# Kernel tuning notes

Hardware: AMD Instinct MI355X
Metric: run time of the kernel (lower is better)

## Reference

```python
import jax, jax.numpy as jnp
import numpy as np

B, L, H = 32, 2048, 512
EPS = 1e-6


def setup_inputs() -> dict:
    key = jax.random.key(0)
    k1, k2 = jax.random.split(key)
    hidden = jax.random.normal(k1, (B, L, H), dtype=jnp.float32)
    # nn.Linear(H, H): weight [H, H], bias [H]; use kaiming-uniform-like scale
    bound = 1.0 / np.sqrt(H)
    W = jax.random.uniform(k2, (H, H), dtype=jnp.float32, minval=-bound, maxval=bound)
    b = jnp.zeros((H,), dtype=jnp.float32)
    return {"hidden": hidden, "W": W, "b": b}


def reference(hidden, W, b):
    Bn, Ln, Hn = hidden.shape

    def step(M, k):
        # k: [B, H]; key == value == hidden[:, t, :]
        v_pred = jnp.einsum("bij,bj->bi", M, k)               # M @ k
        denom = jnp.sum(k * k, axis=-1, keepdims=True) + EPS   # [B, 1]
        delta_v = k - v_pred / denom                           # v - v_pred/denom (v == k)
        M = M + jnp.einsum("bi,bj->bij", delta_v, k)           # outer-product update
        return M, None

    M0 = jnp.zeros((Bn, Hn, Hn), dtype=hidden.dtype)
    xs = jnp.swapaxes(hidden[:, :-1, :], 0, 1)  # [L-1, B, H]
    M, _ = jax.lax.scan(step, M0, xs)

    query = hidden[:, -1, :]                                   # [B, H]
    context = jnp.einsum("bij,bj->bi", M, query)               # [B, H]
    return context @ W.T + b                                   # read_proj
```

## Files before the change

kernel.cpp:

```cpp
#include <hip/hip_runtime.h>
#include <hip/hip_fp16.h>

#define B_  32
#define L_  2048
#define H_  512
#define CA  64
#define NC  32
#define EPSF 1e-6f

typedef _Float16 f16x8 __attribute__((ext_vector_type(8)));
typedef float f32x16 __attribute__((ext_vector_type(16)));

template <int CTRL>
__device__ __forceinline__ float dpp_shift_add(float x) {
  int t = __builtin_amdgcn_update_dpp(0, __float_as_int(x), CTRL, 0xf, 0xf, true);
  return x + __int_as_float(t);
}
__device__ __forceinline__ float wave_reduce_lane63(float x) {
  x = dpp_shift_add<0x111>(x);
  x = dpp_shift_add<0x112>(x);
  x = dpp_shift_add<0x114>(x);
  x = dpp_shift_add<0x118>(x);
  x = dpp_shift_add<0x142>(x);
  x = dpp_shift_add<0x143>(x);
  return x;
}
__device__ __forceinline__ float row16_reduce(float x) {
  x = dpp_shift_add<0x111>(x);
  x = dpp_shift_add<0x112>(x);
  x = dpp_shift_add<0x114>(x);
  x = dpp_shift_add<0x118>(x);
  return x;
}
__device__ __forceinline__ float rdlane(float v, int l) {
  return __int_as_float(__builtin_amdgcn_readlane(__float_as_int(v), l));
}
__device__ __forceinline__ void unpack8(const uint4& k, float* f) {
  const float2 f0 = __half22float2(*(const __half2*)&k.x);
  const float2 f1 = __half22float2(*(const __half2*)&k.y);
  const float2 f2 = __half22float2(*(const __half2*)&k.z);
  const float2 f3 = __half22float2(*(const __half2*)&k.w);
  f[0] = f0.x; f[1] = f0.y; f[2] = f1.x; f[3] = f1.y;
  f[4] = f2.x; f[5] = f2.y; f[6] = f3.x; f[7] = f3.y;
}

#define KFI(row, k8) (((((row) * 64) + (k8)) * 8) ^ (((row) & 7) << 3))

__global__ __launch_bounds__(256) void
deltarule_gram64(const float* __restrict__ hidden,
                 unsigned short* __restrict__ Kh,
                 float* __restrict__ tmT, float* __restrict__ dvec) {
  const int cb = blockIdx.x, b = blockIdx.y;
  const int tid = threadIdx.x, lane = tid & 63, wv = tid >> 6;
  __shared__ __align__(16) unsigned short Kf[CA * H_];
  __shared__ __align__(16) float G[CA * CA];

  const int c0 = cb * CA;
  const float* src = hidden + ((size_t)b * L_ + c0) * H_;
  unsigned short* kout = Kh + ((size_t)b * L_ + c0) * H_;
  const bool lastc = (cb == NC - 1);

#pragma unroll
  for (int u = 0; u < 16; ++u) {
    const int f8 = u * 256 + tid;
    const int row = f8 >> 6;
    const int colf = (f8 & 63) * 8;
    float4 va = *(const float4*)(src + row * H_ + colf);
    float4 vb = *(const float4*)(src + row * H_ + colf + 4);
    if (lastc && row == CA - 1) {
      va = make_float4(0.f, 0.f, 0.f, 0.f);
      vb = make_float4(0.f, 0.f, 0.f, 0.f);
    }
    __half2 h0 = __floats2half2_rn(va.x, va.y);
    __half2 h1 = __floats2half2_rn(va.z, va.w);
    __half2 h2 = __floats2half2_rn(vb.x, vb.y);
    __half2 h3 = __floats2half2_rn(vb.z, vb.w);
    uint4 pk = make_uint4(*(unsigned int*)&h0, *(unsigned int*)&h1,
                          *(unsigned int*)&h2, *(unsigned int*)&h3);
    *(uint4*)&Kf[KFI(row, colf >> 3)] = pk;
    *(uint4*)(kout + row * H_ + colf) = pk;
  }
  __syncthreads();

  if (wv < 3) {
    const int ta = (wv == 2) ? 1 : 0;
    const int tb = (wv == 0) ? 0 : 1;
    const int mrow = 32 * ta + (lane & 31);
    const int nrow = 32 * tb + (lane & 31);
    const int khi = lane >> 5;
    f32x16 acc;
#pragma unroll
    for (int r = 0; r < 16; ++r) acc[r] = 0.f;
#pragma unroll
    for (int kk = 0; kk < 32; ++kk) {
      const int k8 = 2 * kk + khi;
      const f16x8 av = *(const f16x8*)&Kf[KFI(mrow, k8)];
      const f16x8 bv = *(const f16x8*)&Kf[KFI(nrow, k8)];
      acc = __builtin_amdgcn_mfma_f32_32x32x16_f16(av, bv, acc, 0, 0, 0);
    }
#pragma unroll
    for (int r = 0; r < 16; ++r) {
      const int row32 = (r & 3) + 8 * (r >> 2) + 4 * khi;
      G[(32 * ta + row32) * CA + 32 * tb + (lane & 31)] = acc[r];
    }
  }
  __syncthreads();

  if (tid < CA) dvec[((size_t)b * NC + cb) * CA + tid] = G[tid * CA + tid] + EPSF;
  __syncthreads();

  if (wv < 2) {
    const int off = wv * 32;
    const int j = lane & 31;
    float Gr[32], X[32];
#pragma unroll
    for (int t = 0; t < 32; ++t) Gr[t] = G[(off + t) * CA + off + j];
#pragma unroll
    for (int t = 31; t >= 0; --t) {
      float i0 = 0.f, i1 = 0.f;
#pragma unroll
      for (int s = t + 1; s < 32; s += 2) i0 = fmaf(rdlane(Gr[t], s), X[s], i0);
#pragma unroll
      for (int s = t + 2; s < 32; s += 2) i1 = fmaf(rdlane(Gr[t], s), X[s], i1);
      X[t] = (((j == t) ? 1.f : 0.f) - (i0 + i1)) / (rdlane(Gr[t], t) + EPSF);
    }
    if (lane < 32) {
#pragma unroll
      for (int t = 0; t < 32; ++t) G[(off + t) * CA + off + j] = X[t];
    }
  }
  __syncthreads();

  const int zr = tid >> 3;
  const int zc = (tid & 7) * 4;
  float4 zf = make_float4(0.f, 0.f, 0.f, 0.f);
#pragma unroll
  for (int s = 0; s < 32; ++s) {
    const float u = G[zr * CA + 32 + s];
    const float4 xv = *(const float4*)&G[(32 + s) * CA + 32 + zc];
    zf.x = fmaf(u, xv.x, zf.x); zf.y = fmaf(u, xv.y, zf.y);
    zf.z = fmaf(u, xv.z, zf.z); zf.w = fmaf(u, xv.w, zf.w);
  }
  __syncthreads();
  *(float4*)&G[zr * CA + 32 + zc] = zf;
  __syncthreads();
  float4 yf = make_float4(0.f, 0.f, 0.f, 0.f);
#pragma unroll
  for (int s = 0; s < 32; ++s) {
    const float u = G[zr * CA + s];
    const float4 zv = *(const float4*)&G[s * CA + 32 + zc];
    yf.x = fmaf(u, zv.x, yf.x); yf.y = fmaf(u, zv.y, yf.y);
    yf.z = fmaf(u, zv.z, yf.z); yf.w = fmaf(u, zv.w, yf.w);
  }
  __syncthreads();
  *(float4*)&G[zr * CA + 32 + zc] = make_float4(-yf.x, -yf.y, -yf.z, -yf.w);
  __syncthreads();

  float* tout = tmT + ((size_t)b * NC + cb) * (CA * CA);
#pragma unroll
  for (int v = 0; v < 4; ++v) {
    const int f4 = v * 256 + tid;
    const int s = f4 >> 4;
    const int j4 = (f4 & 15) * 4;
    float4 val;
    if (s >= 32 && j4 < 32) val = make_float4(0.f, 0.f, 0.f, 0.f);
    else                    val = *(const float4*)&G[s * CA + j4];
    *(float4*)(tout + s * CA + j4) = val;
  }
}

__global__ __launch_bounds__(1024) void
deltarule_scan64p(const float* __restrict__ hidden,
                  const unsigned short* __restrict__ Kh,
                  const float* __restrict__ Wm, const float* __restrict__ bias,
                  const float* __restrict__ tmT, const float* __restrict__ dvec,
                  float* __restrict__ out) {
  const int b = blockIdx.x, tid = threadIdx.x, lane = tid & 63, wv = tid >> 6;
  __shared__ __align__(16) float Wsw[H_];
  __shared__ __align__(16) float Ctx[H_];
  __shared__ __align__(16) float PartU[16 * 1024];
  __shared__ float Part2[64 * 17];

  const unsigned short* khb = Kh + (size_t)b * L_ * H_;
  const float* tmb = tmT + (size_t)b * NC * (CA * CA);
  const float* dvb = dvec + (size_t)b * NC * CA;

  const int job = 64 * wv + lane;

  if (tid < H_) {
    const float q = hidden[((size_t)b * L_ + (L_ - 1)) * H_ + tid];
    const int p = ((tid & 4) << 6) + ((tid >> 3) << 2) + (tid & 3);
    Wsw[p] = q;
  }
  float4 wq4 = make_float4(0.f, 0.f, 0.f, 0.f);
  float4 cq4 = make_float4(0.f, 0.f, 0.f, 0.f);
  if (wv < 2)
    wq4 = *(const float4*)(hidden + ((size_t)b * L_ + (L_ - 1)) * H_ + 4 * job);

  int cmbBase = 0;
  if (wv < 2)                 cmbBase = (job & 1) * 256 + (job >> 1) * 4;
  else if (wv < 4) { const int qc = job - 128;
                     cmbBase = 512 + (qc & 1) * 256 + (qc >> 1) * 4; }

  uint4 kr[4];
  float4 tA;
  float dv;
#pragma unroll
  for (int i = 0; i < 4; ++i)
    kr[i] = *(const uint4*)(khb + ((size_t)(NC - 1) * CA + 4 * wv + i) * H_ + 8 * lane);
  tA = *(const float4*)(tmb + (size_t)(NC - 1) * (CA * CA) + lane * CA + 4 * wv);
  dv = dvb[(NC - 1) * CA + lane];
  asm volatile("s_waitcnt vmcnt(0) lgkmcnt(0)\n\ts_barrier" ::: "memory");

  for (int c = NC - 1; c >= 0; --c) {
    uint4 kn[4];
    float4 nA;
    float dN = 0.f;
    if (c > 0) {
#pragma unroll
      for (int i = 0; i < 4; ++i)
        kn[i] = *(const uint4*)(khb + ((size_t)(c - 1) * CA + 4 * wv + i) * H_ + 8 * lane);
      nA = *(const float4*)(tmb + (size_t)(c - 1) * (CA * CA) + lane * CA + 4 * wv);
      dN = dvb[(c - 1) * CA + lane];
    }

    const float4 wa  = *(const float4*)&Wsw[4 * lane];
    const float4 wb2 = *(const float4*)&Wsw[256 + 4 * lane];
    float ysg[4];
#pragma unroll
    for (int i = 0; i < 4; ++i) {
      float kf[8];
      unpack8(kr[i], kf);
      float p = kf[0] * wa.x;
      p = fmaf(kf[1], wa.y, p);  p = fmaf(kf[2], wa.z, p);
      p = fmaf(kf[3], wa.w, p);  p = fmaf(kf[4], wb2.x, p);
      p = fmaf(kf[5], wb2.y, p); p = fmaf(kf[6], wb2.z, p);
      p = fmaf(kf[7], wb2.w, p);
      p = wave_reduce_lane63(p);
      ysg[i] = rdlane(p, 63);
    }

    float sp = ysg[0] * tA.x;
    sp = fmaf(ysg[1], tA.y, sp);
    sp = fmaf(ysg[2], tA.z, sp);
    sp = fmaf(ysg[3], tA.w, sp);
    Part2[lane * 17 + wv] = sp;
    asm volatile("s_waitcnt lgkmcnt(0)\n\ts_barrier" ::: "memory");

    float red = Part2[(4 * wv + (lane >> 4)) * 17 + (lane & 15)];
    red = row16_reduce(red);
    const float sg0 = rdlane(red, 15);
    const float sg1 = rdlane(red, 31);
    const float sg2 = rdlane(red, 47);
    const float sg3 = rdlane(red, 63);
    const float sv0 = sg0 * rdlane(dv, 4 * wv + 0);
    const float sv1 = sg1 * rdlane(dv, 4 * wv + 1);
    const float sv2 = sg2 * rdlane(dv, 4 * wv + 2);
    const float sv3 = sg3 * rdlane(dv, 4 * wv + 3);

    float ws[8] = {0,0,0,0,0,0,0,0}, cs[8] = {0,0,0,0,0,0,0,0};
#pragma unroll
    for (int i = 0; i < 4; ++i) {
      float kf[8];
      unpack8(kr[i], kf);
      const float sg = (i == 0) ? sg0 : (i == 1) ? sg1 : (i == 2) ? sg2 : sg3;
      const float sv = (i == 0) ? sv0 : (i == 1) ? sv1 : (i == 2) ? sv2 : sv3;
#pragma unroll
      for (int e = 0; e < 8; ++e) {
        ws[e] = fmaf(sg, kf[e], ws[e]);
        cs[e] = fmaf(sv, kf[e], cs[e]);
      }
    }
    {
      float* pw = &PartU[wv * 1024];
      *(float4*)&pw[4 * lane]       = make_float4(ws[0], ws[1], ws[2], ws[3]);
      *(float4*)&pw[256 + 4 * lane] = make_float4(ws[4], ws[5], ws[6], ws[7]);
      *(float4*)&pw[512 + 4 * lane] = make_float4(cs[0], cs[1], cs[2], cs[3]);
      *(float4*)&pw[768 + 4 * lane] = make_float4(cs[4], cs[5], cs[6], cs[7]);
    }
    asm volatile("s_waitcnt lgkmcnt(0)\n\ts_barrier" ::: "memory");

    if (wv < 4) {
      float4 s = make_float4(0.f, 0.f, 0.f, 0.f);
#pragma unroll
      for (int w2 = 0; w2 < 16; ++w2) {
        const float4 p4 = *(const float4*)&PartU[w2 * 1024 + cmbBase];
        s.x += p4.x; s.y += p4.y; s.z += p4.z; s.w += p4.w;
      }
      if (wv < 2) {
        wq4.x -= s.x; wq4.y -= s.y; wq4.z -= s.z; wq4.w -= s.w;
        *(float4*)&Wsw[256 * (job & 1) + 4 * (job >> 1)] = wq4;
      } else {
        cq4.x += s.x; cq4.y += s.y; cq4.z += s.z; cq4.w += s.w;
      }
    }

    if (c > 0) {
      dv = dN; tA = nA;
#pragma unroll
      for (int i = 0; i < 4; ++i) kr[i] = kn[i];
    }
    asm volatile("s_waitcnt vmcnt(0) lgkmcnt(0)\n\ts_barrier" ::: "memory");
  }

  if (wv == 2 || wv == 3) {
    const int qc = job - 128;
    *(float4*)&Ctx[4 * qc] = cq4;
  }
  __syncthreads();
  {
    const int o = tid & (H_ - 1);
    const int hf = tid >> 9;
    float acc = 0.f;
    const float* wr = Wm + (size_t)o * H_ + hf * 256;
    const float* cx = &Ctx[hf * 256];
#pragma unroll 8
    for (int i = 0; i < 256; i += 4) {
      const float4 w4 = *(const float4*)(wr + i);
      const float4 cv = *(const float4*)(cx + i);
      acc = fmaf(w4.x, cv.x, acc); acc = fmaf(w4.y, cv.y, acc);
      acc = fmaf(w4.z, cv.z, acc); acc = fmaf(w4.w, cv.w, acc);
    }
    PartU[hf * 512 + o] = acc;
  }
  __syncthreads();
  if (tid < H_) out[(size_t)b * H_ + tid] = PartU[tid] + PartU[512 + tid] + bias[tid];
}

extern "C" void kernel_launch(void* const* d_in, const int* in_sizes, int n_in,
                              void* d_out, int out_size, void* d_ws, size_t ws_size,
                              hipStream_t stream) {
  (void)in_sizes; (void)n_in; (void)out_size; (void)ws_size;
  const float* hidden = (const float*)d_in[0];
  const float* Wm     = (const float*)d_in[1];
  const float* bias   = (const float*)d_in[2];
  float* out = (float*)d_out;

  const size_t szKh = (size_t)B_ * L_ * H_ * sizeof(unsigned short);
  unsigned short* Kh = (unsigned short*)d_ws;
  float* tmT  = (float*)((char*)d_ws + szKh);
  float* dvec = tmT + (size_t)B_ * NC * CA * CA;

  deltarule_gram64<<<dim3(NC, B_), 256, 0, stream>>>(hidden, Kh, tmT, dvec);
  deltarule_scan64p<<<B_, 1024, 0, stream>>>(hidden, Kh, Wm, bias, tmT, dvec, out);
}
```

Measured before the change: 343.2 us.

## Store chunk transform in fp16 and stage half of key rows via async LDS loads

The gram kernel now writes the per-chunk T matrix as clamped fp16 instead of fp32, halving that buffer's traffic. The scan kernel keeps only half of each chunk's key rows in registers. The other half is prefetched through double-buffered global_load_lds into shared memory, and the wave-to-row mapping changes to match. This is meant to cut register pressure and global load latency on the serial chunk loop, at the cost of extra LDS traffic and some reduced precision in T.

```diff
diff --git a/kernel.cpp b/kernel.cpp
--- a/kernel.cpp
+++ b/kernel.cpp
@@ -43,13 +43,21 @@
   f[0] = f0.x; f[1] = f0.y; f[2] = f1.x; f[3] = f1.y;
   f[4] = f2.x; f[5] = f2.y; f[6] = f3.x; f[7] = f3.y;
 }
+__device__ __forceinline__ float clamp16(float v) {
+  return fminf(fmaxf(v, -65504.f), 65504.f);
+}
+__device__ __forceinline__ void load_lds16h(const unsigned short* g, unsigned short* l) {
+  __builtin_amdgcn_global_load_lds(
+      (const __attribute__((address_space(1))) unsigned int*)(g),
+      (__attribute__((address_space(3))) unsigned int*)(l), 16, 0, 0);
+}
 
 #define KFI(row, k8) (((((row) * 64) + (k8)) * 8) ^ (((row) & 7) << 3))
 
 __global__ __launch_bounds__(256) void
 deltarule_gram64(const float* __restrict__ hidden,
                  unsigned short* __restrict__ Kh,
-                 float* __restrict__ tmT, float* __restrict__ dvec) {
+                 unsigned short* __restrict__ tmh, float* __restrict__ dvec) {
   const int cb = blockIdx.x, b = blockIdx.y;
   const int tid = threadIdx.x, lane = tid & 63, wv = tid >> 6;
   __shared__ __align__(16) unsigned short Kf[CA * H_];
@@ -156,7 +164,7 @@
   *(float4*)&G[zr * CA + 32 + zc] = make_float4(-yf.x, -yf.y, -yf.z, -yf.w);
   __syncthreads();
 
-  float* tout = tmT + ((size_t)b * NC + cb) * (CA * CA);
+  unsigned short* tout = tmh + ((size_t)b * NC + cb) * (CA * CA);
 #pragma unroll
   for (int v = 0; v < 4; ++v) {
     const int f4 = v * 256 + tid;
@@ -165,24 +173,28 @@
     float4 val;
     if (s >= 32 && j4 < 32) val = make_float4(0.f, 0.f, 0.f, 0.f);
     else                    val = *(const float4*)&G[s * CA + j4];
-    *(float4*)(tout + s * CA + j4) = val;
+    const __half2 a  = __floats2half2_rn(clamp16(val.x), clamp16(val.y));
+    const __half2 bb = __floats2half2_rn(clamp16(val.z), clamp16(val.w));
+    const uint2 pk = make_uint2(*(const unsigned int*)&a, *(const unsigned int*)&bb);
+    *(uint2*)(tout + s * CA + j4) = pk;
   }
 }
 
 __global__ __launch_bounds__(1024) void
-deltarule_scan64p(const float* __restrict__ hidden,
+deltarule_scan64d(const float* __restrict__ hidden,
                   const unsigned short* __restrict__ Kh,
                   const float* __restrict__ Wm, const float* __restrict__ bias,
-                  const float* __restrict__ tmT, const float* __restrict__ dvec,
+                  const unsigned short* __restrict__ tmh, const float* __restrict__ dvec,
                   float* __restrict__ out) {
   const int b = blockIdx.x, tid = threadIdx.x, lane = tid & 63, wv = tid >> 6;
+  __shared__ __align__(16) unsigned short KL[2][32 * H_];
   __shared__ __align__(16) float Wsw[H_];
   __shared__ __align__(16) float Ctx[H_];
   __shared__ __align__(16) float PartU[16 * 1024];
   __shared__ float Part2[64 * 17];
 
   const unsigned short* khb = Kh + (size_t)b * L_ * H_;
-  const float* tmb = tmT + (size_t)b * NC * (CA * CA);
+  const unsigned short* tmb = tmh + (size_t)b * NC * (CA * CA);
   const float* dvb = dvec + (size_t)b * NC * CA;
 
   const int job = 64 * wv + lane;
@@ -202,35 +214,60 @@
   else if (wv < 4) { const int qc = job - 128;
                      cmbBase = 512 + (qc & 1) * 256 + (qc >> 1) * 4; }
 
-  uint4 kr[4];
-  float4 tA;
+  {
+    const unsigned short* s0 = khb + ((size_t)(NC - 1) * CA + 32) * H_;
+#pragma unroll
+    for (int u = 0; u < 2; ++u) {
+      const int off = (u * 16 + wv) * 512;
+      load_lds16h(s0 + off + 8 * lane, &KL[(NC - 1) & 1][off]);
+    }
+  }
+  uint4 kr[2];
+  float2 x01, x23;
   float dv;
-#pragma unroll
-  for (int i = 0; i < 4; ++i)
-    kr[i] = *(const uint4*)(khb + ((size_t)(NC - 1) * CA + 4 * wv + i) * H_ + 8 * lane);
-  tA = *(const float4*)(tmb + (size_t)(NC - 1) * (CA * CA) + lane * CA + 4 * wv);
-  dv = dvb[(NC - 1) * CA + lane];
+  {
+#pragma unroll
+    for (int i = 0; i < 2; ++i)
+      kr[i] = *(const uint4*)(khb + ((size_t)(NC - 1) * CA + 2 * wv + i) * H_ + 8 * lane);
+    const unsigned short* tp = tmb + (size_t)(NC - 1) * (CA * CA) + lane * CA;
+    x01 = __half22float2(*(const __half2*)&tp[2 * wv]);
+    x23 = __half22float2(*(const __half2*)&tp[32 + 2 * wv]);
+    dv = dvb[(NC - 1) * CA + lane];
+  }
   asm volatile("s_waitcnt vmcnt(0) lgkmcnt(0)\n\ts_barrier" ::: "memory");
 
   for (int c = NC - 1; c >= 0; --c) {
-    uint4 kn[4];
-    float4 nA;
+    const int buf = c & 1;
+
+    uint4 kn[2];
+    float2 nx01, nx23;
     float dN = 0.f;
     if (c > 0) {
 #pragma unroll
-      for (int i = 0; i < 4; ++i)
-        kn[i] = *(const uint4*)(khb + ((size_t)(c - 1) * CA + 4 * wv + i) * H_ + 8 * lane);
-      nA = *(const float4*)(tmb + (size_t)(c - 1) * (CA * CA) + lane * CA + 4 * wv);
+      for (int i = 0; i < 2; ++i)
+        kn[i] = *(const uint4*)(khb + ((size_t)(c - 1) * CA + 2 * wv + i) * H_ + 8 * lane);
+      const unsigned short* tp = tmb + (size_t)(c - 1) * (CA * CA) + lane * CA;
+      nx01 = __half22float2(*(const __half2*)&tp[2 * wv]);
+      nx23 = __half22float2(*(const __half2*)&tp[32 + 2 * wv]);
       dN = dvb[(c - 1) * CA + lane];
+      const unsigned short* s1 = khb + ((size_t)(c - 1) * CA + 32) * H_;
+#pragma unroll
+      for (int u = 0; u < 2; ++u) {
+        const int off = (u * 16 + wv) * 512;
+        load_lds16h(s1 + off + 8 * lane, &KL[buf ^ 1][off]);
+      }
     }
 
     const float4 wa  = *(const float4*)&Wsw[4 * lane];
     const float4 wb2 = *(const float4*)&Wsw[256 + 4 * lane];
+    uint4 klr[2];
+    klr[0] = *(const uint4*)&KL[buf][(2 * wv + 0) * H_ + 8 * lane];
+    klr[1] = *(const uint4*)&KL[buf][(2 * wv + 1) * H_ + 8 * lane];
     float ysg[4];
 #pragma unroll
     for (int i = 0; i < 4; ++i) {
       float kf[8];
-      unpack8(kr[i], kf);
+      unpack8((i < 2) ? kr[i] : klr[i - 2], kf);
       float p = kf[0] * wa.x;
       p = fmaf(kf[1], wa.y, p);  p = fmaf(kf[2], wa.z, p);
       p = fmaf(kf[3], wa.w, p);  p = fmaf(kf[4], wb2.x, p);
@@ -240,38 +277,40 @@
       ysg[i] = rdlane(p, 63);
     }
 
-    float sp = ysg[0] * tA.x;
-    sp = fmaf(ysg[1], tA.y, sp);
-    sp = fmaf(ysg[2], tA.z, sp);
-    sp = fmaf(ysg[3], tA.w, sp);
+    float sp = ysg[0] * x01.x;
+    sp = fmaf(ysg[1], x01.y, sp);
+    sp = fmaf(ysg[2], x23.x, sp);
+    sp = fmaf(ysg[3], x23.y, sp);
     Part2[lane * 17 + wv] = sp;
     asm volatile("s_waitcnt lgkmcnt(0)\n\ts_barrier" ::: "memory");
 
-    float red = Part2[(4 * wv + (lane >> 4)) * 17 + (lane & 15)];
-    red = row16_reduce(red);
-    const float sg0 = rdlane(red, 15);
-    const float sg1 = rdlane(red, 31);
-    const float sg2 = rdlane(red, 47);
-    const float sg3 = rdlane(red, 63);
-    const float sv0 = sg0 * rdlane(dv, 4 * wv + 0);
-    const float sv1 = sg1 * rdlane(dv, 4 * wv + 1);
-    const float sv2 = sg2 * rdlane(dv, 4 * wv + 2);
-    const float sv3 = sg3 * rdlane(dv, 4 * wv + 3);
-
-    float ws[8] = {0,0,0,0,0,0,0,0}, cs[8] = {0,0,0,0,0,0,0,0};
-#pragma unroll
-    for (int i = 0; i < 4; ++i) {
-      float kf[8];
-      unpack8(kr[i], kf);
-      const float sg = (i == 0) ? sg0 : (i == 1) ? sg1 : (i == 2) ? sg2 : sg3;
-      const float sv = (i == 0) ? sv0 : (i == 1) ? sv1 : (i == 2) ? sv2 : sv3;
-#pragma unroll
-      for (int e = 0; e < 8; ++e) {
-        ws[e] = fmaf(sg, kf[e], ws[e]);
-        cs[e] = fmaf(sv, kf[e], cs[e]);
+    {
+      const int g = lane >> 4;
+      const int rowg = 2 * wv + (g & 1) + 32 * (g >> 1);
+      float red = Part2[rowg * 17 + (lane & 15)];
+      red = row16_reduce(red);
+      const float sg0 = rdlane(red, 15);
+      const float sg1 = rdlane(red, 31);
+      const float sg2 = rdlane(red, 47);
+      const float sg3 = rdlane(red, 63);
+      const float sv0 = sg0 * rdlane(dv, 2 * wv + 0);
+      const float sv1 = sg1 * rdlane(dv, 2 * wv + 1);
+      const float sv2 = sg2 * rdlane(dv, 32 + 2 * wv);
+      const float sv3 = sg3 * rdlane(dv, 33 + 2 * wv);
+
+      float ws[8] = {0,0,0,0,0,0,0,0}, cs[8] = {0,0,0,0,0,0,0,0};
+#pragma unroll
+      for (int i = 0; i < 4; ++i) {
+        float kf[8];
+        unpack8((i < 2) ? kr[i] : klr[i - 2], kf);
+        const float sg = (i == 0) ? sg0 : (i == 1) ? sg1 : (i == 2) ? sg2 : sg3;
+        const float sv = (i == 0) ? sv0 : (i == 1) ? sv1 : (i == 2) ? sv2 : sv3;
+#pragma unroll
+        for (int e = 0; e < 8; ++e) {
+          ws[e] = fmaf(sg, kf[e], ws[e]);
+          cs[e] = fmaf(sv, kf[e], cs[e]);
+        }
       }
-    }
-    {
       float* pw = &PartU[wv * 1024];
       *(float4*)&pw[4 * lane]       = make_float4(ws[0], ws[1], ws[2], ws[3]);
       *(float4*)&pw[256 + 4 * lane] = make_float4(ws[4], ws[5], ws[6], ws[7]);
@@ -296,9 +335,8 @@
     }
 
     if (c > 0) {
-      dv = dN; tA = nA;
-#pragma unroll
-      for (int i = 0; i < 4; ++i) kr[i] = kn[i];
+      dv = dN; x01 = nx01; x23 = nx23;
+      kr[0] = kn[0]; kr[1] = kn[1];
     }
     asm volatile("s_waitcnt vmcnt(0) lgkmcnt(0)\n\ts_barrier" ::: "memory");
   }
@@ -337,10 +375,11 @@
   float* out = (float*)d_out;
 
   const size_t szKh = (size_t)B_ * L_ * H_ * sizeof(unsigned short);
-  unsigned short* Kh = (unsigned short*)d_ws;
-  float* tmT  = (float*)((char*)d_ws + szKh);
-  float* dvec = tmT + (size_t)B_ * NC * CA * CA;
-
-  deltarule_gram64<<<dim3(NC, B_), 256, 0, stream>>>(hidden, Kh, tmT, dvec);
-  deltarule_scan64p<<<B_, 1024, 0, stream>>>(hidden, Kh, Wm, bias, tmT, dvec, out);
-}
+  const size_t szTm = (size_t)B_ * NC * CA * CA * sizeof(unsigned short);
+  unsigned short* Kh  = (unsigned short*)d_ws;
+  unsigned short* tmh = (unsigned short*)((char*)d_ws + szKh);
+  float* dvec = (float*)((char*)d_ws + szKh + szTm);
+
+  deltarule_gram64<<<dim3(NC, B_), 256, 0, stream>>>(hidden, Kh, tmh, dvec);
+  deltarule_scan64d<<<B_, 1024, 0, stream>>>(hidden, Kh, Wm, bias, tmh, dvec, out);
+}
```

After: 362.5 us. 1.06x slower.
